# Optimization experiments

Hardware: AMD Instinct MI355X
Metric: run time of the kernel (lower is better)

Reference implementation:

```python
import jax, jax.numpy as jnp
import numpy as np

B_NW, N, DIM, NH, DH, HID, NW, WH = 2048, 64, 512, 16, 32, 384, 64, 8
EPS = 1e-12  # F.normalize eps

def _rel_coords_log(wh, ww):
    # torch.cartesian_prod order: i (rows) outer, j (cols) inner
    ii, jj = np.meshgrid(np.arange(wh), np.arange(ww), indexing='ij')
    coords = np.stack([ii.ravel(), jj.ravel()], axis=-1).astype(np.float32)  # [N,2]
    rel = coords[:, None, :] - coords[None, :, :]                            # [N,N,2]
    return (np.sign(rel) * np.log1p(np.abs(rel))).astype(np.float32)

def setup_inputs() -> dict:
    key = jax.random.key(0)
    ks = jax.random.split(key, 9)
    s = 0.02
    inner = NH * DH
    return {
        'x': jax.random.normal(ks[0], (B_NW, N, DIM), jnp.float32),
        'mask': jax.random.normal(ks[1], (NW, N, N), jnp.float32),
        'w_qkv': jax.random.normal(ks[2], (DIM, 3 * inner), jnp.float32) * s,
        'tau': jnp.ones((1, NH, 1, 1), jnp.float32),
        'mlp_w1': jax.random.normal(ks[3], (2, HID), jnp.float32) * s,
        'mlp_b1': jnp.zeros((HID,), jnp.float32),
        'mlp_w2': jax.random.normal(ks[4], (HID, NH), jnp.float32) * s,
        'mlp_b2': jnp.zeros((NH,), jnp.float32),
        'w_out': jax.random.normal(ks[5], (inner, DIM), jnp.float32) * s,
        'b_out': jnp.zeros((DIM,), jnp.float32),
        'rel_log': jnp.asarray(_rel_coords_log(WH, WH)),
    }

def reference(x, mask, w_qkv, tau, mlp_w1, mlp_b1, mlp_w2, mlp_b2, w_out, b_out, rel_log):
    b, n, _ = x.shape
    qkv = x @ w_qkv                                   # [b, n, 3*nh*dh]
    qkv = qkv.reshape(b, n, 3, NH, DH)
    q, k, v = (jnp.transpose(qkv[:, :, i], (0, 2, 1, 3)) for i in range(3))  # [b, nh, n, dh]
    # cosine attention: L2-normalize q and k along head dim
    q = q / jnp.maximum(jnp.linalg.norm(q, axis=-1, keepdims=True), EPS)
    k = k / jnp.maximum(jnp.linalg.norm(k, axis=-1, keepdims=True), EPS)
    sim = jnp.einsum('bhid,bhjd->bhij', q, k) * tau   # learned temperature
    # relative position bias via meta MLP: [N,N,2] -> [N,N,nh]
    bias = jax.nn.relu(rel_log @ mlp_w1 + mlp_b1) @ mlp_w2 + mlp_b2
    sim = sim + jnp.transpose(bias, (2, 0, 1))[None]  # [1, nh, N, N]
    nw = mask.shape[0]
    sim = sim.reshape(b // nw, nw, NH, n, n) + mask[None, :, None]
    sim = sim.reshape(b, NH, n, n)
    attn = jax.nn.softmax(sim, axis=-1)
    out = jnp.einsum('bhij,bhjd->bhid', attn, v)
    out = jnp.transpose(out, (0, 2, 1, 3)).reshape(b, n, NH * DH)
    return out @ w_out + b_out
```

## Files before the change

### kernel.cpp

```cpp
#include <hip/hip_runtime.h>
#include <hip/hip_bf16.h>


typedef __bf16 bf16;
typedef __bf16 v4bf __attribute__((ext_vector_type(4)));
typedef __bf16 v8bf __attribute__((ext_vector_type(8)));
typedef float  v4f  __attribute__((ext_vector_type(4)));

__device__ __forceinline__ int swzA(int o) { return o ^ (((o >> 10) & 7) << 4); }

__global__ void convert_w_kernel(const float* __restrict__ wqkv, const float* __restrict__ wout,
                                 bf16* __restrict__ Wt, bf16* __restrict__ WoT) {
    int idx = blockIdx.x * 256 + threadIdx.x;
    Wt[idx] = (bf16)wqkv[(idx & 511) * 1536 + (idx >> 9)];
    if (idx < 262144) WoT[idx] = (bf16)wout[(idx & 511) * 512 + (idx >> 9)];
}

__global__ void bias_kernel(const float* __restrict__ rel_log, const float* __restrict__ w1,
                            const float* __restrict__ b1, const float* __restrict__ w2,
                            const float* __restrict__ b2, float* __restrict__ bias) {
    int p = blockIdx.x * 256 + threadIdx.x;
    float ra = rel_log[p * 2 + 0];
    float rb = rel_log[p * 2 + 1];
    float acc[16];
    #pragma unroll
    for (int t = 0; t < 16; ++t) acc[t] = 0.f;
    for (int kk = 0; kk < 384; ++kk) {
        float hv = fmaxf(ra * w1[kk] + rb * w1[384 + kk] + b1[kk], 0.f);
        #pragma unroll
        for (int t = 0; t < 16; ++t) acc[t] += hv * w2[kk * 16 + t];
    }
    #pragma unroll
    for (int t = 0; t < 16; ++t) bias[t * 4096 + p] = acc[t] + b2[t];
}

__global__ void comb_kernel(const float* __restrict__ bias, const float* __restrict__ mask,
                            float* __restrict__ comb) {
    int idx = blockIdx.x * 256 + threadIdx.x;
    int t = idx & 4095, wh = idx >> 12;
    int w = wh >> 4, h = wh & 15;
    int ji = t >> 8, rem = t & 255;
    int j = ji >> 2, i = ji & 3;
    int q16 = rem >> 2, r = t & 3;
    int lq = q16 >> 4, lm = q16 & 15;
    int p = (i * 16 + lm) * 64 + j * 16 + lq * 4 + r;
    comb[idx] = bias[h * 4096 + p] + mask[w * 4096 + p];
}

__global__ __launch_bounds__(512, 4) void qkv_fused_kernel(
    const float* __restrict__ x,
    const bf16* __restrict__ Wt,
    bf16* __restrict__ q_ws, bf16* __restrict__ k_ws, bf16* __restrict__ v_ws)
{
    __shared__ alignas(16) char Albuf[65536];
    const int mb = blockIdx.x;
    const int t = threadIdx.x;
    const int wv = t >> 6, lane = t & 63, lq = lane >> 4, lm = lane & 15;

    {
        const char* xbase = (const char*)x + (size_t)mb * 64 * 2048;
        #pragma unroll
        for (int p = 0; p < 8; ++p) {
            int o = p * 8192 + t * 16;
            const float4* src = (const float4*)(xbase + (size_t)o * 2);
            float4 f0 = src[0], f1 = src[1];
            v8bf a = { (bf16)f0.x, (bf16)f0.y, (bf16)f0.z, (bf16)f0.w,
                       (bf16)f1.x, (bf16)f1.y, (bf16)f1.z, (bf16)f1.w };
            *(v8bf*)(&Albuf[swzA(o)]) = a;
        }
    }
    __syncthreads();

    int abase[4];
    #pragma unroll
    for (int i = 0; i < 4; ++i) {
        int row = i * 16 + lm;
        abase[i] = (row * 1024 + lq * 16) ^ ((row & 7) << 4);
    }

    const int bw = mb;

    #pragma unroll 1
    for (int pass = 0; pass < 3; ++pass) {
        const bf16* bBase = Wt + (size_t)(pass * 512 + wv * 64) * 512;

        v4f acc[4][4];
        #pragma unroll
        for (int i = 0; i < 4; ++i)
            #pragma unroll
            for (int j = 0; j < 4; ++j) acc[i][j] = v4f{0.f, 0.f, 0.f, 0.f};

        #pragma unroll 4
        for (int kt = 0; kt < 16; ++kt) {
            v8bf af[4], bfj[4];
            #pragma unroll
            for (int j = 0; j < 4; ++j)
                bfj[j] = *(const v8bf*)(bBase + (size_t)(j * 16 + lm) * 512 + kt * 32 + lq * 8);
            #pragma unroll
            for (int i = 0; i < 4; ++i)
                af[i] = *(const v8bf*)(&Albuf[abase[i] ^ (kt << 6)]);
            #pragma unroll
            for (int i = 0; i < 4; ++i)
                #pragma unroll
                for (int j = 0; j < 4; ++j)
                    acc[i][j] = __builtin_amdgcn_mfma_f32_16x16x32_bf16(af[i], bfj[j], acc[i][j], 0, 0, 0);
        }

        if (pass < 2) {
            bf16* dst = (pass == 0) ? q_ws : k_ws;
            #pragma unroll
            for (int j = 0; j < 4; ++j) {
                const int h = wv * 2 + (j >> 1);
                const int dcol = (j & 1) * 16 + lm;
                #pragma unroll
                for (int i = 0; i < 4; ++i)
                    #pragma unroll
                    for (int r = 0; r < 4; ++r) {
                        int n = i * 16 + lq * 4 + r;
                        dst[((size_t)(bw * 16 + h) * 64 + n) * 32 + dcol] = (bf16)acc[i][j][r];
                    }
            }
        } else {
            #pragma unroll
            for (int j = 0; j < 4; ++j) {
                const int h = wv * 2 + (j >> 1);
                const int dh = (j & 1) * 16 + lm;
                #pragma unroll
                for (int i = 0; i < 4; ++i) {
                    v4bf pv = { (bf16)acc[i][j][0], (bf16)acc[i][j][1],
                                (bf16)acc[i][j][2], (bf16)acc[i][j][3] };
                    *(v4bf*)(v_ws + ((size_t)(bw * 16 + h) * 32 + dh) * 64 + i * 16 + lq * 4) = pv;
                }
            }
        }
    }
}

__global__ __launch_bounds__(512) void attn_proj_kernel(
    const bf16* __restrict__ q_ws,
    const bf16* __restrict__ k_ws,
    const bf16* __restrict__ v_ws,
    const float* __restrict__ comb,
    const float* __restrict__ tau,
    const bf16* __restrict__ WoT,
    const float* __restrict__ b_out,
    int wofs,
    float* __restrict__ out)
{
    __shared__ alignas(16) bf16 AO[64 * 520];
    __shared__ alignas(16) bf16 P_all[8][64 * 72];
    const int b = blockIdx.x;
    const int tid = threadIdx.x;
    const int wv = tid >> 6, lane = tid & 63, lq = lane >> 4, lm = lane & 15;
    const v4f z4 = {0.f, 0.f, 0.f, 0.f};
    bf16* P = P_all[wv];

    #pragma unroll 1
    for (int hh = 0; hh < 2; ++hh) {
        const int h = wv * 2 + hh;
        const size_t qk_base = (size_t)(b * 16 + h) * 64 * 32;
        const float* comb_hw = comb + ((size_t)(((wofs + b) & 63) * 16 + h)) * 4096
                                    + (lq * 16 + lm) * 4;
        const float tau_h = tau[h];

        v8bf qf[4], kf[4];
        #pragma unroll
        for (int i = 0; i < 4; ++i)
            qf[i] = *(const v8bf*)(q_ws + qk_base + (i * 16 + lm) * 32 + lq * 8);
        #pragma unroll
        for (int j = 0; j < 4; ++j)
            kf[j] = *(const v8bf*)(k_ws + qk_base + (j * 16 + lm) * 32 + lq * 8);

        #pragma unroll
        for (int i = 0; i < 4; ++i) {
            float a = 0.f;
            #pragma unroll
            for (int e = 0; e < 8; ++e) { float f = (float)qf[i][e]; a = fmaf(f, f, a); }
            a += __shfl_xor(a, 16); a += __shfl_xor(a, 32);
            float sc = tau_h / fmaxf(sqrtf(a), 1e-12f);
            #pragma unroll
            for (int e = 0; e < 8; ++e) qf[i][e] = (bf16)((float)qf[i][e] * sc);
        }
        #pragma unroll
        for (int j = 0; j < 4; ++j) {
            float a = 0.f;
            #pragma unroll
            for (int e = 0; e < 8; ++e) { float f = (float)kf[j][e]; a = fmaf(f, f, a); }
            a += __shfl_xor(a, 16); a += __shfl_xor(a, 32);
            float sc = 1.0f / fmaxf(sqrtf(a), 1e-12f);
            #pragma unroll
            for (int e = 0; e < 8; ++e) kf[j][e] = (bf16)((float)kf[j][e] * sc);
        }

        v4f st[4][4];
        #pragma unroll
        for (int j = 0; j < 4; ++j)
            #pragma unroll
            for (int i = 0; i < 4; ++i)
                st[j][i] = __builtin_amdgcn_mfma_f32_16x16x32_bf16(kf[j], qf[i], z4, 0, 0, 0);

        #pragma unroll
        for (int j = 0; j < 4; ++j)
            #pragma unroll
            for (int i = 0; i < 4; ++i) {
                float4 cv = *(const float4*)(comb_hw + (j * 4 + i) * 256);
                st[j][i][0] += cv.x; st[j][i][1] += cv.y;
                st[j][i][2] += cv.z; st[j][i][3] += cv.w;
            }

        #pragma unroll
        for (int i = 0; i < 4; ++i) {
            float mx = st[0][i][0];
            #pragma unroll
            for (int j = 0; j < 4; ++j)
                #pragma unroll
                for (int r = 0; r < 4; ++r) mx = fmaxf(mx, st[j][i][r]);
            mx = fmaxf(mx, __shfl_xor(mx, 16));
            mx = fmaxf(mx, __shfl_xor(mx, 32));
            float sm = 0.f;
            #pragma unroll
            for (int j = 0; j < 4; ++j)
                #pragma unroll
                for (int r = 0; r < 4; ++r) {
                    float e = __expf(st[j][i][r] - mx);
                    st[j][i][r] = e; sm += e;
                }
            sm += __shfl_xor(sm, 16); sm += __shfl_xor(sm, 32);
            float rcp = 1.0f / sm;
            #pragma unroll
            for (int j = 0; j < 4; ++j) {
                v4bf pv = { (bf16)(st[j][i][0] * rcp), (bf16)(st[j][i][1] * rcp),
                            (bf16)(st[j][i][2] * rcp), (bf16)(st[j][i][3] * rcp) };
                *(v4bf*)(P + (i * 16 + lm) * 72 + j * 16 + lq * 4) = pv;
            }
        }

        const size_t v_base = (size_t)(b * 16 + h) * 32 * 64;
        v4f o[4][2];
        #pragma unroll
        for (int i = 0; i < 4; ++i)
            #pragma unroll
            for (int nt = 0; nt < 2; ++nt) o[i][nt] = z4;
        #pragma unroll
        for (int kk = 0; kk < 2; ++kk) {
            v8bf vf[2], pf[4];
            #pragma unroll
            for (int nt = 0; nt < 2; ++nt)
                vf[nt] = *(const v8bf*)(v_ws + v_base + (nt * 16 + lm) * 64 + kk * 32 + lq * 8);
            #pragma unroll
            for (int i = 0; i < 4; ++i)
                pf[i] = *(const v8bf*)(P + (i * 16 + lm) * 72 + kk * 32 + lq * 8);
            #pragma unroll
            for (int i = 0; i < 4; ++i)
                #pragma unroll
                for (int nt = 0; nt < 2; ++nt)
                    o[i][nt] = __builtin_amdgcn_mfma_f32_16x16x32_bf16(pf[i], vf[nt], o[i][nt], 0, 0, 0);
        }
        #pragma unroll
        for (int i = 0; i < 4; ++i)
            #pragma unroll
            for (int nt = 0; nt < 2; ++nt)
                #pragma unroll
                for (int r = 0; r < 4; ++r)
                    AO[(i * 16 + lq * 4 + r) * 520 + h * 32 + nt * 16 + lm] = (bf16)o[i][nt][r];
    }

    __syncthreads();

    v4f acc[4][4];
    #pragma unroll
    for (int i = 0; i < 4; ++i)
        #pragma unroll
        for (int j = 0; j < 4; ++j) acc[i][j] = v4f{0.f, 0.f, 0.f, 0.f};

    #pragma unroll 2
    for (int kc = 0; kc < 16; ++kc) {
        v8bf af[4], bfj[4];
        #pragma unroll
        for (int j = 0; j < 4; ++j)
            bfj[j] = *(const v8bf*)(WoT + (size_t)(wv * 64 + j * 16 + lm) * 512 + kc * 32 + lq * 8);
        #pragma unroll
        for (int i = 0; i < 4; ++i)
            af[i] = *(const v8bf*)(AO + (i * 16 + lm) * 520 + kc * 32 + lq * 8);
        #pragma unroll
        for (int i = 0; i < 4; ++i)
            #pragma unroll
            for (int j = 0; j < 4; ++j)
                acc[i][j] = __builtin_amdgcn_mfma_f32_16x16x32_bf16(af[i], bfj[j], acc[i][j], 0, 0, 0);
    }

    #pragma unroll
    for (int j = 0; j < 4; ++j) {
        const int col = wv * 64 + j * 16 + lm;
        const float bo = b_out[col];
        #pragma unroll
        for (int i = 0; i < 4; ++i)
            #pragma unroll
            for (int r = 0; r < 4; ++r)
                out[(size_t)(b * 64 + i * 16 + lq * 4 + r) * 512 + col] = acc[i][j][r] + bo;
    }
}

extern "C" void kernel_launch(void* const* d_in, const int* in_sizes, int n_in,
                              void* d_out, int out_size, void* d_ws, size_t ws_size,
                              hipStream_t stream) {
    (void)in_sizes; (void)n_in; (void)out_size;
    const float* x       = (const float*)d_in[0];
    const float* mask    = (const float*)d_in[1];
    const float* w_qkv   = (const float*)d_in[2];
    const float* tau     = (const float*)d_in[3];
    const float* mlp_w1  = (const float*)d_in[4];
    const float* mlp_b1  = (const float*)d_in[5];
    const float* mlp_w2  = (const float*)d_in[6];
    const float* mlp_b2  = (const float*)d_in[7];
    const float* w_out   = (const float*)d_in[8];
    const float* b_out   = (const float*)d_in[9];
    const float* rel_log = (const float*)d_in[10];
    float* out = (float*)d_out;

    char* ws = (char*)d_ws;
    bf16*  Wt     = (bf16*)(ws);
    bf16*  WoT    = (bf16*)(ws + 1572864);
    float* bias   = (float*)(ws + 2097152);
    float* comb   = (float*)(ws + 2359296);
    char*  qkv_base = ws + 19136512;

    size_t avail = (ws_size > 19136512ULL) ? ws_size - 19136512ULL : 0;
    int W = 2048;
    while (W > 128 && (size_t)W * 196608ULL > avail) W >>= 1;
    const size_t qkbuf = (size_t)W * 65536;
    bf16* qb = (bf16*)qkv_base;
    bf16* kb = (bf16*)(qkv_base + qkbuf);
    bf16* vb = (bf16*)(qkv_base + 2 * qkbuf);

    convert_w_kernel<<<3072, 256, 0, stream>>>(w_qkv, w_out, Wt, WoT);
    bias_kernel<<<16, 256, 0, stream>>>(rel_log, mlp_w1, mlp_b1, mlp_w2, mlp_b2, bias);
    comb_kernel<<<16384, 256, 0, stream>>>(bias, mask, comb);

    const int nchunk = 2048 / W;
    for (int c = 0; c < nchunk; ++c) {
        const float* xc = x + (size_t)c * W * 64 * 512;
        qkv_fused_kernel<<<W, 512, 0, stream>>>(xc, Wt, qb, kb, vb);
        attn_proj_kernel<<<W, 512, 0, stream>>>(qb, kb, vb, comb, tau, WoT, b_out,
                                                c * W, out + (size_t)c * W * 64 * 512);
    }
}
```

Baseline: 783.0 us.

## Double-buffer QKV weight tiles in LDS via async global-to-LDS loads

In the QKV projection kernel, each wave now prefetches its slice of the bf16 weight matrix into a private, swizzled, double-buffered LDS region using global_load_lds. The three passes and sixteen k-steps are flattened into one 48-step loop, with explicit vmcnt waits so the next tile's load overlaps the current MFMAs. Before, each k-step read the B fragments straight from global memory. The extra 64KB of LDS, together with launch bounds relaxed to one block, lowers how many blocks can share a CU. The hand-written waitcnt also makes correctness depend on the count of outstanding memory operations, including the epilogue stores.

```diff
diff --git a/kernel.cpp b/kernel.cpp
--- a/kernel.cpp
+++ b/kernel.cpp
@@ -7,7 +7,11 @@
 typedef __bf16 v8bf __attribute__((ext_vector_type(8)));
 typedef float  v4f  __attribute__((ext_vector_type(4)));
 
+#define AS1 __attribute__((address_space(1)))
+#define AS3 __attribute__((address_space(3)))
+
 __device__ __forceinline__ int swzA(int o) { return o ^ (((o >> 10) & 7) << 4); }
+__device__ __forceinline__ int swzB(int o) { return o ^ (((o >> 7) & 3) << 4); }
 
 __global__ void convert_w_kernel(const float* __restrict__ wqkv, const float* __restrict__ wout,
                                  bf16* __restrict__ Wt, bf16* __restrict__ WoT) {
@@ -47,12 +51,13 @@
     comb[idx] = bias[h * 4096 + p] + mask[w * 4096 + p];
 }
 
-__global__ __launch_bounds__(512, 4) void qkv_fused_kernel(
+__global__ __launch_bounds__(512, 1) void qkv_fused_kernel(
     const float* __restrict__ x,
     const bf16* __restrict__ Wt,
     bf16* __restrict__ q_ws, bf16* __restrict__ k_ws, bf16* __restrict__ v_ws)
 {
     __shared__ alignas(16) char Albuf[65536];
+    __shared__ alignas(16) char Blbuf[8][2][4096];
     const int mb = blockIdx.x;
     const int t = threadIdx.x;
     const int wv = t >> 6, lane = t & 63, lq = lane >> 4, lm = lane & 15;
@@ -69,69 +74,94 @@
             *(v8bf*)(&Albuf[swzA(o)]) = a;
         }
     }
+
+    auto stageB = [&](int buf, int pass, int kt) {
+        const char* bBase = (const char*)Wt + (size_t)(pass * 512 + wv * 64) * 1024;
+        char* dst = &Blbuf[wv][buf][0];
+        #pragma unroll
+        for (int p = 0; p < 4; ++p) {
+            int o = p * 1024 + lane * 16;
+            int s = swzB(o);
+            __builtin_amdgcn_global_load_lds(
+                (const AS1 void*)(bBase + (size_t)(s >> 6) * 1024 + kt * 64 + (s & 63)),
+                (AS3 void*)(dst + o), 16, 0, 0);
+        }
+    };
+
+    stageB(0, 0, 0);
     __syncthreads();
 
-    int abase[4];
+    int abase[4], boff[4];
     #pragma unroll
     for (int i = 0; i < 4; ++i) {
-        int row = i * 16 + lm;
-        abase[i] = (row * 1024 + lq * 16) ^ ((row & 7) << 4);
+        int arow = i * 16 + lm;
+        abase[i] = (arow * 1024 + lq * 16) ^ ((arow & 7) << 4);
+        int brow = i * 16 + lm;
+        boff[i] = (brow * 64) + (((lq ^ (brow >> 1)) & 3) * 16);
     }
 
     const int bw = mb;
+    v4f acc[4][4];
+    #pragma unroll
+    for (int i = 0; i < 4; ++i)
+        #pragma unroll
+        for (int j = 0; j < 4; ++j) acc[i][j] = v4f{0.f, 0.f, 0.f, 0.f};
 
     #pragma unroll 1
-    for (int pass = 0; pass < 3; ++pass) {
-        const bf16* bBase = Wt + (size_t)(pass * 512 + wv * 64) * 512;
-
-        v4f acc[4][4];
-        #pragma unroll
-        for (int i = 0; i < 4; ++i)
-            #pragma unroll
-            for (int j = 0; j < 4; ++j) acc[i][j] = v4f{0.f, 0.f, 0.f, 0.f};
-
-        #pragma unroll 4
-        for (int kt = 0; kt < 16; ++kt) {
-            v8bf af[4], bfj[4];
+    for (int ph = 0; ph < 48; ++ph) {
+        const int pass = ph >> 4, kt = ph & 15;
+        if (ph < 47) {
+            const int nph = ph + 1;
+            stageB(nph & 1, nph >> 4, nph & 15);
+            asm volatile("s_waitcnt vmcnt(4)" ::: "memory");
+        } else {
+            asm volatile("s_waitcnt vmcnt(0)" ::: "memory");
+        }
+        __builtin_amdgcn_sched_barrier(0);
+        const char* Bb = &Blbuf[wv][ph & 1][0];
+        v8bf af[4], bfj[4];
+        #pragma unroll
+        for (int j = 0; j < 4; ++j) bfj[j] = *(const v8bf*)(Bb + boff[j]);
+        #pragma unroll
+        for (int i = 0; i < 4; ++i) af[i] = *(const v8bf*)(&Albuf[abase[i] ^ (kt << 6)]);
+        #pragma unroll
+        for (int i = 0; i < 4; ++i)
             #pragma unroll
             for (int j = 0; j < 4; ++j)
-                bfj[j] = *(const v8bf*)(bBase + (size_t)(j * 16 + lm) * 512 + kt * 32 + lq * 8);
-            #pragma unroll
-            for (int i = 0; i < 4; ++i)
-                af[i] = *(const v8bf*)(&Albuf[abase[i] ^ (kt << 6)]);
-            #pragma unroll
-            for (int i = 0; i < 4; ++i)
-                #pragma unroll
-                for (int j = 0; j < 4; ++j)
-                    acc[i][j] = __builtin_amdgcn_mfma_f32_16x16x32_bf16(af[i], bfj[j], acc[i][j], 0, 0, 0);
-        }
-
-        if (pass < 2) {
-            bf16* dst = (pass == 0) ? q_ws : k_ws;
-            #pragma unroll
-            for (int j = 0; j < 4; ++j) {
-                const int h = wv * 2 + (j >> 1);
-                const int dcol = (j & 1) * 16 + lm;
-                #pragma unroll
-                for (int i = 0; i < 4; ++i)
+                acc[i][j] = __builtin_amdgcn_mfma_f32_16x16x32_bf16(af[i], bfj[j], acc[i][j], 0, 0, 0);
+
+        if (kt == 15) {
+            if (pass < 2) {
+                bf16* dst = (pass == 0) ? q_ws : k_ws;
+                #pragma unroll
+                for (int j = 0; j < 4; ++j) {
+                    const int h = wv * 2 + (j >> 1);
+                    const int dcol = (j & 1) * 16 + lm;
                     #pragma unroll
-                    for (int r = 0; r < 4; ++r) {
-                        int n = i * 16 + lq * 4 + r;
-                        dst[((size_t)(bw * 16 + h) * 64 + n) * 32 + dcol] = (bf16)acc[i][j][r];
+                    for (int i = 0; i < 4; ++i)
+                        #pragma unroll
+                        for (int r = 0; r < 4; ++r) {
+                            int n = i * 16 + lq * 4 + r;
+                            dst[((size_t)(bw * 16 + h) * 64 + n) * 32 + dcol] = (bf16)acc[i][j][r];
+                        }
+                }
+            } else {
+                #pragma unroll
+                for (int j = 0; j < 4; ++j) {
+                    const int h = wv * 2 + (j >> 1);
+                    const int dh = (j & 1) * 16 + lm;
+                    #pragma unroll
+                    for (int i = 0; i < 4; ++i) {
+                        v4bf pv = { (bf16)acc[i][j][0], (bf16)acc[i][j][1],
+                                    (bf16)acc[i][j][2], (bf16)acc[i][j][3] };
+                        *(v4bf*)(v_ws + ((size_t)(bw * 16 + h) * 32 + dh) * 64 + i * 16 + lq * 4) = pv;
                     }
-            }
-        } else {
-            #pragma unroll
-            for (int j = 0; j < 4; ++j) {
-                const int h = wv * 2 + (j >> 1);
-                const int dh = (j & 1) * 16 + lm;
-                #pragma unroll
-                for (int i = 0; i < 4; ++i) {
-                    v4bf pv = { (bf16)acc[i][j][0], (bf16)acc[i][j][1],
-                                (bf16)acc[i][j][2], (bf16)acc[i][j][3] };
-                    *(v4bf*)(v_ws + ((size_t)(bw * 16 + h) * 32 + dh) * 64 + i * 16 + lq * 4) = pv;
                 }
             }
+            #pragma unroll
+            for (int i = 0; i < 4; ++i)
+                #pragma unroll
+                for (int j = 0; j < 4; ++j) acc[i][j] = v4f{0.f, 0.f, 0.f, 0.f};
         }
     }
 }
```

Result: faster. 693.3 us (-11.4%).
